# Performance work log

Measured on AMD Instinct MI355X. Metric: run time of the kernel, lower is better.

## Reference

```python
import jax, jax.numpy as jnp
import numpy as np

K, NR, NT, D, NLAYER = 128, 1, 128, 1, 8
PMAX = float(np.power(10.0, 10.0 / 10.0))  # snr=10 dB
SIGMA = 1.0


def _cx(x):
    # [2, ...] real/imag-stacked -> complex
    return x[0] + 1j * x[1]


def _ct(x):
    # conjugate transpose on last two axes
    return jnp.conj(jnp.swapaxes(x, -1, -2))


def _layer(Vc, Hc, up1, up3, up4, wp1, wp3, vp1, vp2, vp4):
    # Vc: [K,Nt,d] complex, Hc: [K,Nr,Nt] complex; params complex, batched over K.
    cdt = Vc.dtype
    I_nr = jnp.eye(NR, dtype=cdt)
    I_d = jnp.eye(D, dtype=cdt)
    I_nt = jnp.eye(NT, dtype=cdt)
    # ---- A_update: A_i = sigma/Pmax * sum_j tr(V_j V_j^H) * I + H_i (sum_j V_j V_j^H) H_i^H
    tr_vv = jnp.einsum('knd,knd->', Vc, jnp.conj(Vc))          # complex scalar
    S = jnp.einsum('knd,kmd->nm', Vc, jnp.conj(Vc))            # [Nt,Nt]
    A = (SIGMA / PMAX) * tr_vv * I_nr + jnp.einsum('krt,tm,ksm->krs', Hc, S, jnp.conj(Hc))  # [K,Nr,Nr]
    # ---- U layer: A_inv_i = p1_i inv(A_i) + 0.01 p3_i ; U_i = A_inv_i H_i V_i + p4_i
    A_inv = up1 @ jnp.linalg.inv(A) + 0.01 * up3
    Un = A_inv @ Hc @ Vc + up4                                  # [K,Nr,d]
    # ---- E_update: E_i = I - U_i^H H_i V_i
    E = I_d - _ct(Un) @ Hc @ Vc                                 # [K,d,d]
    # ---- W layer: W_i = 0.1 p1_i inv(E_i) + 0.01 p3_i
    Wn = 0.1 * (wp1 @ jnp.linalg.inv(E)) + 0.01 * wp3           # [K,d,d]
    # ---- B_update: B = sigma/Pmax * sum_i tr(U_i W_i U_i^H) * I + sum_i H_i^H U_i W_i U_i^H H_i (same for all users)
    UWU = Un @ Wn @ _ct(Un)                                     # [K,Nr,Nr]
    tr_uwu = jnp.trace(UWU, axis1=-2, axis2=-1).sum()
    B = (SIGMA / PMAX) * tr_uwu * I_nt + jnp.sum(_ct(Hc) @ UWU @ Hc, axis=0)  # [Nt,Nt]
    B_inv = jnp.linalg.inv(B)
    # ---- V
    if vp2 is None:  # FinalV: V_i = inv(B) H_i^H U_i W_i
        Vn = (B_inv @ _ct(Hc)) @ Un @ Wn
    else:            # V layer: B_inv_i = p2_i inv(B) + 0.01 p4_i ; V_i = B_inv_i H_i^H U_i W_i + p1_i
        Bm = vp2 @ B_inv + 0.01 * vp4
        Vn = Bm @ _ct(Hc) @ Un @ Wn + vp1
    # ---- Normalize: scale by sqrt(Pmax)/sqrt(Re sum_j tr(V_j V_j^H))
    pw = jnp.sqrt(jnp.real(jnp.einsum('knd,knd->', Vn, jnp.conj(Vn))))
    return (jnp.sqrt(PMAX) / pw) * Vn


def setup_inputs() -> dict:
    key = jax.random.key(0)
    ks = jax.random.split(key, 20)
    f32 = jnp.float32
    def rn(k, shape, scale):
        return (scale * jax.random.normal(k, shape)).astype(f32)
    inp = {
        'V': rn(ks[0], (2, K, NT, D), 1.0),
        'H': rn(ks[1], (2, K, NR, NT), 1.0),
        # mid-layer params, stacked over layers: only params actually used in forward
        'mid_u_p1': rn(ks[2], (NLAYER, 2, K, NR, NR), 0.001),
        'mid_u_p3': rn(ks[3], (NLAYER, 2, K, NR, NR), 0.01),
        'mid_u_p4': rn(ks[4], (NLAYER, 2, K, NR, D), 0.01),
        'mid_w_p1': rn(ks[5], (NLAYER, 2, K, D, D), 0.001),
        'mid_w_p3': rn(ks[6], (NLAYER, 2, K, D, D), 0.01),
        'mid_v_p1': rn(ks[7], (NLAYER, 2, K, NT, D), 0.001),
        'mid_v_p2': rn(ks[8], (NLAYER, 2, K, NT, NT), 0.01),
        'mid_v_p4': rn(ks[9], (NLAYER, 2, K, NT, NT), 0.01),
        # final layer (U + W only)
        'fin_u_p1': rn(ks[10], (2, K, NR, NR), 0.001),
        'fin_u_p3': rn(ks[11], (2, K, NR, NR), 0.01),
        'fin_u_p4': rn(ks[12], (2, K, NR, D), 0.01),
        'fin_w_p1': rn(ks[13], (2, K, D, D), 0.001),
        'fin_w_p3': rn(ks[14], (2, K, D, D), 0.01),
    }
    return inp


def reference(V, H, mid_u_p1, mid_u_p3, mid_u_p4, mid_w_p1, mid_w_p3,
              mid_v_p1, mid_v_p2, mid_v_p4,
              fin_u_p1, fin_u_p3, fin_u_p4, fin_w_p1, fin_w_p3):
    Vc = _cx(V)
    Hc = _cx(H)
    n = mid_u_p1.shape[0]
    for l in range(n):
        Vc = _layer(Vc, Hc,
                    _cx(mid_u_p1[l]), _cx(mid_u_p3[l]), _cx(mid_u_p4[l]),
                    _cx(mid_w_p1[l]), _cx(mid_w_p3[l]),
                    _cx(mid_v_p1[l]), _cx(mid_v_p2[l]), _cx(mid_v_p4[l]))
    Vc = _layer(Vc, Hc,
                _cx(fin_u_p1), _cx(fin_u_p3), _cx(fin_u_p4),
                _cx(fin_w_p1), _cx(fin_w_p3), None, None, None)
    return jnp.stack([jnp.real(Vc), jnp.imag(Vc)]).astype(jnp.float32)
```

## Files before the change

kernel.cpp:

```cpp
#include <hip/hip_runtime.h>
#include <math.h>

#define KK 128
#define NTT 128
#define PMAXF 10.0f
#define SP 0.1f
#define LUT 512
#define LDA 129

typedef float2 c32;

__device__ __forceinline__ c32 cmul(c32 a, c32 b){
    return make_float2(a.x*b.x - a.y*b.y, a.x*b.y + a.y*b.x);
}
__device__ __forceinline__ c32 cmulc(c32 a, c32 b){
    return make_float2(a.x*b.x + a.y*b.y, a.y*b.x - a.x*b.y);
}
__device__ __forceinline__ c32 cinv(c32 a){
    float d = 1.0f/(a.x*a.x + a.y*a.y);
    return make_float2(a.x*d, -a.y*d);
}

__global__ void k_trvv(const float* __restrict__ V0, float* __restrict__ out){
    float s = 0.f;
    for (int e = blockIdx.x*blockDim.x + threadIdx.x; e < 2*KK*NTT; e += gridDim.x*blockDim.x){
        float v = V0[e]; s += v*v;
    }
    __shared__ float red[4];
    for (int d = 32; d; d >>= 1) s += __shfl_down(s, d);
    int lane = threadIdx.x & 63, w = threadIdx.x >> 6;
    if (!lane) red[w] = s;
    __syncthreads();
    if (!threadIdx.x){
        float t = red[0] + red[1] + red[2] + red[3];
        atomicAdd(out, t);
    }
}

__global__ void k_stage1(const float* __restrict__ Hre, const float* __restrict__ Him,
                         const float* __restrict__ V0re, const float* __restrict__ V0im,
                         const float2* __restrict__ VN, int use_vn,
                         const float* __restrict__ pw2prev,
                         const float* __restrict__ trvvp,
                         const float* __restrict__ u1, const float* __restrict__ u3,
                         const float* __restrict__ u4, const float* __restrict__ w1,
                         const float* __restrict__ w3,
                         float* __restrict__ wre, float* __restrict__ wim,
                         float* __restrict__ sre, float* __restrict__ sim,
                         float* __restrict__ sumw)
{
    int k = blockIdx.x, j = threadIdx.x;
    __shared__ float hre_s[NTT], him_s[NTT];
    __shared__ float redq[NTT];
    __shared__ c32 pkk_s;
    hre_s[j] = Hre[k*NTT + j];
    him_s[j] = Him[k*NTT + j];
    __syncthreads();

    float g = 1.0f;
    if (pw2prev) g = sqrtf(PMAXF / *pw2prev);

    float pre = 0.f, pim = 0.f;
    if (use_vn){
        const float2* vr = VN + j*NTT;
        #pragma unroll 4
        for (int n = 0; n < NTT; n++){
            float2 v = vr[n];
            pre += hre_s[n]*v.x - him_s[n]*v.y;
            pim += hre_s[n]*v.y + him_s[n]*v.x;
        }
    } else {
        const float* vr = V0re + j*NTT;
        const float* vi = V0im + j*NTT;
        #pragma unroll 4
        for (int n = 0; n < NTT; n++){
            float a = vr[n], b = vi[n];
            pre += hre_s[n]*a - him_s[n]*b;
            pim += hre_s[n]*b + him_s[n]*a;
        }
    }
    pre *= g; pim *= g;
    if (j == k) pkk_s = make_float2(pre, pim);
    redq[j] = pre*pre + pim*pim;
    __syncthreads();
    for (int d = 64; d; d >>= 1){
        if (j < d) redq[j] += redq[j + d];
        __syncthreads();
    }
    if (j == 0){
        float trvv = pw2prev ? PMAXF : *trvvp;
        float A = SP*trvv + redq[0];
        float invA = 1.0f/A;
        c32 p1 = make_float2(u1[k], u1[KK + k]);
        c32 p3 = make_float2(u3[k], u3[KK + k]);
        c32 p4 = make_float2(u4[k], u4[KK + k]);
        c32 Ainv = make_float2(p1.x*invA + 0.01f*p3.x, p1.y*invA + 0.01f*p3.y);
        c32 Pkk = pkk_s;
        c32 U = cmul(Ainv, Pkk); U.x += p4.x; U.y += p4.y;
        c32 t = cmulc(Pkk, U);
        c32 E = make_float2(1.0f - t.x, -t.y);
        c32 iE = cinv(E);
        c32 q1 = make_float2(w1[k], w1[KK + k]);
        c32 q3 = make_float2(w3[k], w3[KK + k]);
        c32 W = cmul(q1, iE);
        W.x = 0.1f*W.x + 0.01f*q3.x;
        W.y = 0.1f*W.y + 0.01f*q3.y;
        float u2 = U.x*U.x + U.y*U.y;
        c32 wk = make_float2(u2*W.x, u2*W.y);
        c32 sk = cmul(U, W);
        wre[k] = wk.x; wim[k] = wk.y;
        sre[k] = sk.x; sim[k] = sk.y;
        atomicAdd(&sumw[0], wk.x);
        atomicAdd(&sumw[1], wk.y);
    }
}

__global__ void k_bbuild(const float* __restrict__ Hre, const float* __restrict__ Him,
                         const float* __restrict__ wre, const float* __restrict__ wim,
                         const float* __restrict__ sumw, float2* __restrict__ B)
{
    int n = blockIdx.x, m = threadIdx.x;
    __shared__ float cr[KK], ci[KK];
    {
        int k = m;
        c32 h = make_float2(Hre[k*NTT + n], -Him[k*NTT + n]);
        c32 wk = make_float2(wre[k], wim[k]);
        c32 t = cmul(h, wk);
        cr[k] = t.x; ci[k] = t.y;
    }
    __syncthreads();
    float br = 0.f, bi = 0.f;
    #pragma unroll 4
    for (int k = 0; k < KK; k++){
        float hr = Hre[k*NTT + m], hi = Him[k*NTT + m];
        br += cr[k]*hr - ci[k]*hi;
        bi += cr[k]*hi + ci[k]*hr;
    }
    if (n == m){ br += SP*sumw[0]; bi += SP*sumw[1]; }
    B[n*NTT + m] = make_float2(br, bi);
}

__global__ void __launch_bounds__(512, 1) k_lu3(const float2* __restrict__ B,
                                                float2* __restrict__ BT,
                                                float2* __restrict__ rcg,
                                                int* __restrict__ permg)
{
    extern __shared__ float2 As[];
    __shared__ float2 rc_s[KK];
    __shared__ float2 Msc[112*16];
    int t = threadIdx.x;

    for (int e = t; e < KK*NTT; e += LUT){
        int r = e >> 7, c = e & 127;
        As[r*LDA + c] = B[e];
    }
    __syncthreads();

    for (int j = 0; j < 8; ++j){
        const int J0 = j*16;
        for (int ii = 0; ii < 16; ++ii){
            const int gi = J0 + ii;
            float2 piv = As[gi*LDA + gi];
            float2 rc = cinv(piv);
            if (t == 0) rc_s[gi] = rc;
            const int w = 15 - ii;
            const int nel = (127 - gi) * w;
            for (int e = t; e < nel; e += LUT){
                int r = gi + 1 + e / w;
                int c = gi + 1 + e % w;
                float2 m = cmul(As[r*LDA + gi], rc);
                float2 u = As[gi*LDA + c];
                float2 a = As[r*LDA + c];
                a.x -= m.x*u.x - m.y*u.y;
                a.y -= m.x*u.y + m.y*u.x;
                As[r*LDA + c] = a;
            }
            __syncthreads();
        }
        if (j == 7) break;
        const int T0 = J0 + 16;
        const int Rt = 128 - T0;

        for (int e = t; e < Rt*16; e += LUT){
            int rp = e >> 4, i = e & 15;
            float2 l = As[(T0 + rp)*LDA + J0 + i];
            Msc[rp*16 + i] = cmul(l, rc_s[J0 + i]);
        }
        if (t < Rt){
            int c = T0 + t;
            float2 u[16];
            #pragma unroll
            for (int a2 = 0; a2 < 16; ++a2) u[a2] = As[(J0 + a2)*LDA + c];
            #pragma unroll
            for (int a2 = 1; a2 < 16; ++a2){
                #pragma unroll
                for (int i = 0; i < 16; ++i){
                    if (i < a2){
                        float2 m = cmul(As[(J0 + a2)*LDA + J0 + i], rc_s[J0 + i]);
                        u[a2].x -= m.x*u[i].x - m.y*u[i].y;
                        u[a2].y -= m.x*u[i].y + m.y*u[i].x;
                    }
                }
            }
            #pragma unroll
            for (int a2 = 1; a2 < 16; ++a2) As[(J0 + a2)*LDA + c] = u[a2];
        }
        __syncthreads();

        {
            int cl = t & 127;
            int g  = t >> 7;
            if (cl < Rt){
                int c = T0 + cl;
                float2 u[16];
                #pragma unroll
                for (int i = 0; i < 16; ++i) u[i] = As[(J0 + i)*LDA + c];
                for (int r = T0 + g; r < 128; r += 4){
                    int rp = r - T0;
                    float2 a = As[r*LDA + c];
                    #pragma unroll
                    for (int i = 0; i < 16; ++i){
                        float2 m = Msc[rp*16 + i];
                        a.x -= m.x*u[i].x - m.y*u[i].y;
                        a.y -= m.x*u[i].y + m.y*u[i].x;
                    }
                    As[r*LDA + c] = a;
                }
            }
        }
        __syncthreads();
    }

    for (int e = t; e < KK*NTT; e += LUT){
        int c = e >> 7, r = e & 127;
        BT[e] = As[r*LDA + c];
    }
    if (t < KK){ rcg[t] = rc_s[t]; permg[t] = t; }
}

__global__ void k_solve(const float2* __restrict__ BT, const float2* __restrict__ rcg,
                        const int* __restrict__ permg,
                        const float* __restrict__ Hre, const float* __restrict__ Him,
                        float2* __restrict__ X)
{
    int c = blockIdx.x;
    int lane = threadIdx.x;
    __shared__ float2 rc_s[KK];
    rc_s[lane] = rcg[lane];
    rc_s[lane + 64] = rcg[lane + 64];
    int r0 = lane, r1 = lane + 64;
    int o0 = permg[r0], o1 = permg[r1];
    float2 b0 = make_float2(Hre[c*NTT + o0], -Him[c*NTT + o0]);
    float2 b1 = make_float2(Hre[c*NTT + o1], -Him[c*NTT + o1]);
    __syncthreads();

    float2 cur0[8], cur1[8];
    #pragma unroll
    for (int jj = 0; jj < 8; jj++){ cur0[jj] = BT[jj*NTT + r0]; cur1[jj] = BT[jj*NTT + r1]; }
    for (int ib = 0; ib < 16; ib++){
        float2 n0[8], n1[8];
        if (ib < 15){
            int nb = (ib + 1)*8;
            #pragma unroll
            for (int jj = 0; jj < 8; jj++){ n0[jj] = BT[(nb + jj)*NTT + r0]; n1[jj] = BT[(nb + jj)*NTT + r1]; }
        }
        #pragma unroll
        for (int jj = 0; jj < 8; jj++){
            int i = ib*8 + jj;
            float xr, xi;
            if (i < 64){ xr = __shfl(b0.x, i);      xi = __shfl(b0.y, i); }
            else       { xr = __shfl(b1.x, i - 64); xi = __shfl(b1.y, i - 64); }
            float2 rc = rc_s[i];
            float tr = rc.x*xr - rc.y*xi, ti = rc.x*xi + rc.y*xr;
            float2 l0 = cur0[jj], l1 = cur1[jj];
            if (r0 > i){ b0.x -= l0.x*tr - l0.y*ti; b0.y -= l0.x*ti + l0.y*tr; }
            if (r1 > i){ b1.x -= l1.x*tr - l1.y*ti; b1.y -= l1.x*ti + l1.y*tr; }
        }
        if (ib < 15){
            #pragma unroll
            for (int jj = 0; jj < 8; jj++){ cur0[jj] = n0[jj]; cur1[jj] = n1[jj]; }
        }
    }
    #pragma unroll
    for (int jj = 0; jj < 8; jj++){ cur0[jj] = BT[(120 + jj)*NTT + r0]; cur1[jj] = BT[(120 + jj)*NTT + r1]; }
    for (int ib = 15; ib >= 0; ib--){
        float2 n0[8], n1[8];
        if (ib > 0){
            int nb = (ib - 1)*8;
            #pragma unroll
            for (int jj = 0; jj < 8; jj++){ n0[jj] = BT[(nb + jj)*NTT + r0]; n1[jj] = BT[(nb + jj)*NTT + r1]; }
        }
        #pragma unroll
        for (int jj = 7; jj >= 0; jj--){
            int i = ib*8 + jj;
            float yr, yi;
            if (i < 64){ yr = __shfl(b0.x, i);      yi = __shfl(b0.y, i); }
            else       { yr = __shfl(b1.x, i - 64); yi = __shfl(b1.y, i - 64); }
            float2 rc = rc_s[i];
            float xr = rc.x*yr - rc.y*yi, xi = rc.x*yi + rc.y*yr;
            if (r0 == i){ b0.x = xr; b0.y = xi; }
            if (r1 == i){ b1.x = xr; b1.y = xi; }
            float2 u0 = cur0[jj], u1v = cur1[jj];
            if (r0 < i){ b0.x -= u0.x*xr - u0.y*xi; b0.y -= u0.x*xi + u0.y*xr; }
            if (r1 < i){ b1.x -= u1v.x*xr - u1v.y*xi; b1.y -= u1v.x*xi + u1v.y*xr; }
        }
        if (ib > 0){
            #pragma unroll
            for (int jj = 0; jj < 8; jj++){ cur0[jj] = n0[jj]; cur1[jj] = n1[jj]; }
        }
    }
    X[c*NTT + r0] = b0;
    X[c*NTT + r1] = b1;
}

__global__ void k_matvec(const float* __restrict__ p2re, const float* __restrict__ p2im,
                         const float* __restrict__ p4re, const float* __restrict__ p4im,
                         const float2* __restrict__ X,
                         const float* __restrict__ Hre, const float* __restrict__ Him,
                         float2* __restrict__ Y, float2* __restrict__ Z)
{
    int b = blockIdx.x;
    int k = b >> 1, rh = b & 1;
    int t = threadIdx.x;
    __shared__ float2 xv[NTT], hv[NTT];
    if (t < NTT){
        xv[t] = X[k*NTT + t];
        hv[t] = make_float2(Hre[k*NTT + t], -Him[k*NTT + t]);
    }
    __syncthreads();
    int which = t >> 7, u = t & 127;
    int row = rh*64 + (u >> 1), ch = u & 1;
    size_t base = (size_t)k*16384 + (size_t)row*128 + (size_t)ch*64;
    const float* mre = (which ? p4re : p2re) + base;
    const float* mim = (which ? p4im : p2im) + base;
    const float2* vv = (which ? hv : xv) + ch*64;
    float ar = 0.f, ai = 0.f;
    #pragma unroll 4
    for (int cidx = 0; cidx < 64; cidx++){
        float r_ = mre[cidx], i_ = mim[cidx];
        float2 v = vv[cidx];
        ar += r_*v.x - i_*v.y;
        ai += r_*v.y + i_*v.x;
    }
    ar += __shfl_xor(ar, 1);
    ai += __shfl_xor(ai, 1);
    if (ch == 0){
        (which ? Z : Y)[k*NTT + row] = make_float2(ar, ai);
    }
}

__global__ void k_combine(const float2* __restrict__ Y, const float2* __restrict__ Z,
                          const float* __restrict__ sre, const float* __restrict__ sim,
                          const float* __restrict__ p1re, const float* __restrict__ p1im,
                          float2* __restrict__ VN, float* __restrict__ pw2)
{
    float acc = 0.f;
    for (int e = blockIdx.x*blockDim.x + threadIdx.x; e < KK*NTT; e += gridDim.x*blockDim.x){
        int k = e >> 7;
        c32 s = make_float2(sre[k], sim[k]);
        float2 y = Y[e], z = Z[e];
        y.x += 0.01f*z.x; y.y += 0.01f*z.y;
        c32 v = cmul(s, y);
        v.x += p1re[e]; v.y += p1im[e];
        VN[e] = v;
        acc += v.x*v.x + v.y*v.y;
    }
    __shared__ float red[4];
    for (int d = 32; d; d >>= 1) acc += __shfl_down(acc, d);
    int lane = threadIdx.x & 63, w = threadIdx.x >> 6;
    if (!lane) red[w] = acc;
    __syncthreads();
    if (!threadIdx.x) atomicAdd(pw2, red[0] + red[1] + red[2] + red[3]);
}

__global__ void k_finout(const float2* __restrict__ X,
                         const float* __restrict__ sre, const float* __restrict__ sim,
                         float2* __restrict__ VN, float* __restrict__ pw2)
{
    float acc = 0.f;
    for (int e = blockIdx.x*blockDim.x + threadIdx.x; e < KK*NTT; e += gridDim.x*blockDim.x){
        int k = e >> 7;
        c32 s = make_float2(sre[k], sim[k]);
        c32 v = cmul(s, X[e]);
        VN[e] = v;
        acc += v.x*v.x + v.y*v.y;
    }
    __shared__ float red[4];
    for (int d = 32; d; d >>= 1) acc += __shfl_down(acc, d);
    int lane = threadIdx.x & 63, w = threadIdx.x >> 6;
    if (!lane) red[w] = acc;
    __syncthreads();
    if (!threadIdx.x) atomicAdd(pw2, red[0] + red[1] + red[2] + red[3]);
}

__global__ void k_write(const float2* __restrict__ VN, const float* __restrict__ pw2,
                        float* __restrict__ out)
{
    float gsc = sqrtf(PMAXF / *pw2);
    for (int e = blockIdx.x*blockDim.x + threadIdx.x; e < KK*NTT; e += gridDim.x*blockDim.x){
        float2 v = VN[e];
        out[e] = gsc*v.x;
        out[KK*NTT + e] = gsc*v.y;
    }
}

extern "C" void kernel_launch(void* const* d_in, const int* in_sizes, int n_in,
                              void* d_out, int out_size, void* d_ws, size_t ws_size,
                              hipStream_t stream)
{
    const float* V0  = (const float*)d_in[0];
    const float* H   = (const float*)d_in[1];
    const float* mu1 = (const float*)d_in[2];
    const float* mu3 = (const float*)d_in[3];
    const float* mu4 = (const float*)d_in[4];
    const float* mw1 = (const float*)d_in[5];
    const float* mw3 = (const float*)d_in[6];
    const float* mv1 = (const float*)d_in[7];
    const float* mv2 = (const float*)d_in[8];
    const float* mv4 = (const float*)d_in[9];
    const float* fu1 = (const float*)d_in[10];
    const float* fu3 = (const float*)d_in[11];
    const float* fu4 = (const float*)d_in[12];
    const float* fw1 = (const float*)d_in[13];
    const float* fw3 = (const float*)d_in[14];

    float* ws = (float*)d_ws;
    float*  acc  = ws;
    float*  wre  = ws + 64;
    float*  wim  = ws + 192;
    float*  sre  = ws + 320;
    float*  sim  = ws + 448;
    float2* B    = (float2*)(ws + 1024);
    float2* rc   = (float2*)(ws + 33792);
    int*    perm = (int*)  (ws + 34048);
    float2* X    = (float2*)(ws + 34176);
    float2* Y    = (float2*)(ws + 66944);
    float2* Z    = (float2*)(ws + 99712);
    float2* VN   = (float2*)(ws + 132480);
    float2* BT   = (float2*)(ws + 165248);

    const int LU_LDS = KK*LDA*sizeof(float2);
    (void)hipFuncSetAttribute((const void*)k_lu3,
                              hipFuncAttributeMaxDynamicSharedMemorySize, LU_LDS);

    hipMemsetAsync(ws, 0, 64*sizeof(float), stream);
    k_trvv<<<64, 256, 0, stream>>>(V0, ws + 40);

    const float* Hre = H;
    const float* Him = H + 16384;

    for (int l = 0; l < 9; l++){
        bool fin = (l == 8);
        const float* u1 = fin ? fu1 : mu1 + (size_t)l*256;
        const float* u3 = fin ? fu3 : mu3 + (size_t)l*256;
        const float* u4 = fin ? fu4 : mu4 + (size_t)l*256;
        const float* w1 = fin ? fw1 : mw1 + (size_t)l*256;
        const float* w3 = fin ? fw3 : mw3 + (size_t)l*256;

        k_stage1<<<128, 128, 0, stream>>>(Hre, Him, V0, V0 + 16384, VN, (l > 0) ? 1 : 0,
                                          (l > 0) ? (acc + (l - 1)*4 + 2) : nullptr,
                                          ws + 40,
                                          u1, u3, u4, w1, w3,
                                          wre, wim, sre, sim, acc + l*4);
        k_bbuild<<<128, 128, 0, stream>>>(Hre, Him, wre, wim, acc + l*4, B);
        k_lu3<<<1, 512, LU_LDS, stream>>>(B, BT, rc, perm);
        k_solve<<<128, 64, 0, stream>>>(BT, rc, perm, Hre, Him, X);

        if (!fin){
            const float* p2 = mv2 + (size_t)l*4194304;
            const float* p4 = mv4 + (size_t)l*4194304;
            const float* p1 = mv1 + (size_t)l*32768;
            k_matvec<<<256, 256, 0, stream>>>(p2, p2 + 2097152, p4, p4 + 2097152,
                                              X, Hre, Him, Y, Z);
            k_combine<<<64, 256, 0, stream>>>(Y, Z, sre, sim, p1, p1 + 16384,
                                              VN, acc + l*4 + 2);
        } else {
            k_finout<<<64, 256, 0, stream>>>(X, sre, sim, VN, acc + l*4 + 2);
            k_write<<<64, 256, 0, stream>>>(VN, acc + l*4 + 2, (float*)d_out);
        }
    }
}
```

Baseline: 1.767 ms.

## Overlap p4·H matvec with LU, register-blocked panel LU, fuse matvec with combine

The single-block LU kernel gains 128 extra blocks that compute the independent p4·H^H matvec while block 0 factorises, hiding that bandwidth-bound work behind the serial LU. The LU itself is rewritten: the panel factorisation runs in registers with wave shuffles instead of 16 barrier-separated passes, the U-row triangular update is split across 4 lanes per column with shuffle reductions, and the trailing update uses 4x4 register tiles. The p2·X matvec is fused with the combine and power reduction, removing the Y round trip and one launch. The cost is higher register pressure in the LU block and more complex indexing.

```diff
diff --git a/kernel.cpp b/kernel.cpp
--- a/kernel.cpp
+++ b/kernel.cpp
@@ -140,15 +140,46 @@
     B[n*NTT + m] = make_float2(br, bi);
 }
 
-__global__ void __launch_bounds__(512, 1) k_lu3(const float2* __restrict__ B,
+__global__ void __launch_bounds__(512, 1) k_lu4(const float2* __restrict__ B,
                                                 float2* __restrict__ BT,
                                                 float2* __restrict__ rcg,
-                                                int* __restrict__ permg)
-{
+                                                int* __restrict__ permg,
+                                                const float* __restrict__ p4re,
+                                                const float* __restrict__ p4im,
+                                                const float* __restrict__ Hre,
+                                                const float* __restrict__ Him,
+                                                float2* __restrict__ Z)
+{
+    if (blockIdx.x > 0){
+        int k = blockIdx.x - 1;
+        int t = threadIdx.x;
+        int r = t >> 2, q = t & 3;
+        const float* mre = p4re + (size_t)k*16384 + (size_t)r*128 + q*32;
+        const float* mim = p4im + (size_t)k*16384 + (size_t)r*128 + q*32;
+        const float* hr4 = Hre + k*NTT + q*32;
+        const float* hi4 = Him + k*NTT + q*32;
+        float ar = 0.f, ai = 0.f;
+        #pragma unroll
+        for (int ii = 0; ii < 8; ++ii){
+            float4 a = *(const float4*)(mre + 4*ii);
+            float4 b = *(const float4*)(mim + 4*ii);
+            float4 hr = *(const float4*)(hr4 + 4*ii);
+            float4 hi = *(const float4*)(hi4 + 4*ii);
+            ar += a.x*hr.x + b.x*hi.x;  ai += b.x*hr.x - a.x*hi.x;
+            ar += a.y*hr.y + b.y*hi.y;  ai += b.y*hr.y - a.y*hi.y;
+            ar += a.z*hr.z + b.z*hi.z;  ai += b.z*hr.z - a.z*hi.z;
+            ar += a.w*hr.w + b.w*hi.w;  ai += b.w*hr.w - a.w*hi.w;
+        }
+        ar += __shfl_xor(ar, 1); ai += __shfl_xor(ai, 1);
+        ar += __shfl_xor(ar, 2); ai += __shfl_xor(ai, 2);
+        if (q == 0) Z[k*NTT + r] = make_float2(ar, ai);
+        return;
+    }
+
     extern __shared__ float2 As[];
     __shared__ float2 rc_s[KK];
     __shared__ float2 Msc[112*16];
-    int t = threadIdx.x;
+    const int t = threadIdx.x;
 
     for (int e = t; e < KK*NTT; e += LUT){
         int r = e >> 7, c = e & 127;
@@ -157,74 +188,141 @@
     __syncthreads();
 
     for (int j = 0; j < 8; ++j){
-        const int J0 = j*16;
-        for (int ii = 0; ii < 16; ++ii){
-            const int gi = J0 + ii;
-            float2 piv = As[gi*LDA + gi];
-            float2 rc = cinv(piv);
-            if (t == 0) rc_s[gi] = rc;
-            const int w = 15 - ii;
-            const int nel = (127 - gi) * w;
-            for (int e = t; e < nel; e += LUT){
-                int r = gi + 1 + e / w;
-                int c = gi + 1 + e % w;
-                float2 m = cmul(As[r*LDA + gi], rc);
-                float2 u = As[gi*LDA + c];
-                float2 a = As[r*LDA + c];
-                a.x -= m.x*u.x - m.y*u.y;
-                a.y -= m.x*u.y + m.y*u.x;
-                As[r*LDA + c] = a;
-            }
-            __syncthreads();
-        }
+        const int J0 = j*16, T0 = J0 + 16, Rt = 128 - T0;
+
+        if (t < 64){
+            const int l = t;
+            const int r0 = J0 + l, r1 = J0 + 64 + l;
+            const bool h0 = (r0 < 128), h1 = (r1 < 128);
+            float2 a0[16], a1[16];
+            #pragma unroll
+            for (int c = 0; c < 16; ++c){ a0[c] = make_float2(0.f,0.f); a1[c] = make_float2(0.f,0.f); }
+            if (h0){
+                #pragma unroll
+                for (int c = 0; c < 16; ++c) a0[c] = As[r0*LDA + J0 + c];
+            }
+            if (h1){
+                #pragma unroll
+                for (int c = 0; c < 16; ++c) a1[c] = As[r1*LDA + J0 + c];
+            }
+            #pragma unroll
+            for (int ii = 0; ii < 16; ++ii){
+                float2 piv;
+                piv.x = __shfl(a0[ii].x, ii);
+                piv.y = __shfl(a0[ii].y, ii);
+                float2 rc = cinv(piv);
+                if (l == ii) rc_s[J0 + ii] = rc;
+                float2 m0 = cmul(a0[ii], rc);
+                float2 m1 = cmul(a1[ii], rc);
+                const bool act0 = h0 && (l > ii);
+                #pragma unroll
+                for (int c = ii + 1; c < 16; ++c){
+                    float ux = __shfl(a0[c].x, ii);
+                    float uy = __shfl(a0[c].y, ii);
+                    if (act0){
+                        a0[c].x -= m0.x*ux - m0.y*uy;
+                        a0[c].y -= m0.x*uy + m0.y*ux;
+                    }
+                    if (h1){
+                        a1[c].x -= m1.x*ux - m1.y*uy;
+                        a1[c].y -= m1.x*uy + m1.y*ux;
+                    }
+                }
+            }
+            if (h0){
+                #pragma unroll
+                for (int c = 0; c < 16; ++c) As[r0*LDA + J0 + c] = a0[c];
+            }
+            if (h1){
+                #pragma unroll
+                for (int c = 0; c < 16; ++c) As[r1*LDA + J0 + c] = a1[c];
+            }
+        }
+        __syncthreads();
+
         if (j == 7) break;
-        const int T0 = J0 + 16;
-        const int Rt = 128 - T0;
 
         for (int e = t; e < Rt*16; e += LUT){
             int rp = e >> 4, i = e & 15;
-            float2 l = As[(T0 + rp)*LDA + J0 + i];
-            Msc[rp*16 + i] = cmul(l, rc_s[J0 + i]);
-        }
-        if (t < Rt){
-            int c = T0 + t;
-            float2 u[16];
-            #pragma unroll
-            for (int a2 = 0; a2 < 16; ++a2) u[a2] = As[(J0 + a2)*LDA + c];
-            #pragma unroll
-            for (int a2 = 1; a2 < 16; ++a2){
-                #pragma unroll
-                for (int i = 0; i < 16; ++i){
-                    if (i < a2){
-                        float2 m = cmul(As[(J0 + a2)*LDA + J0 + i], rc_s[J0 + i]);
-                        u[a2].x -= m.x*u[i].x - m.y*u[i].y;
-                        u[a2].y -= m.x*u[i].y + m.y*u[i].x;
+            Msc[e] = cmul(As[(T0 + rp)*LDA + J0 + i], rc_s[J0 + i]);
+        }
+        {
+            int q = t & 3, cidx = t >> 2;
+            if (cidx < Rt){
+                int c = T0 + cidx;
+                float2 uq[4];
+                #pragma unroll
+                for (int kk = 0; kk < 4; ++kk) uq[kk] = As[(J0 + q + 4*kk)*LDA + c];
+                #pragma unroll
+                for (int a2 = 1; a2 < 16; ++a2){
+                    float2 part = make_float2(0.f, 0.f);
+                    #pragma unroll
+                    for (int kk = 0; kk < 4; ++kk){
+                        int i = q + 4*kk;
+                        if (i < a2){
+                            float2 mm = cmul(As[(J0 + a2)*LDA + J0 + i], rc_s[J0 + i]);
+                            float2 p = cmul(mm, uq[kk]);
+                            part.x += p.x; part.y += p.y;
+                        }
+                    }
+                    part.x += __shfl_xor(part.x, 1); part.y += __shfl_xor(part.y, 1);
+                    part.x += __shfl_xor(part.x, 2); part.y += __shfl_xor(part.y, 2);
+                    if (q == (a2 & 3)){
+                        uq[a2 >> 2].x -= part.x;
+                        uq[a2 >> 2].y -= part.y;
                     }
                 }
-            }
-            #pragma unroll
-            for (int a2 = 1; a2 < 16; ++a2) As[(J0 + a2)*LDA + c] = u[a2];
+                #pragma unroll
+                for (int kk = 0; kk < 4; ++kk){
+                    int i = q + 4*kk;
+                    if (i != 0) As[(J0 + i)*LDA + c] = uq[kk];
+                }
+            }
         }
         __syncthreads();
 
         {
-            int cl = t & 127;
-            int g  = t >> 7;
-            if (cl < Rt){
-                int c = T0 + cl;
-                float2 u[16];
-                #pragma unroll
-                for (int i = 0; i < 16; ++i) u[i] = As[(J0 + i)*LDA + c];
-                for (int r = T0 + g; r < 128; r += 4){
-                    int rp = r - T0;
-                    float2 a = As[r*LDA + c];
+            int rt = t & 31, cw = t >> 5;
+            if (rt < (Rt >> 2)){
+                int r0 = T0 + rt*4;
+                float2 m[4][16];
+                #pragma unroll
+                for (int s = 0; s < 4; ++s){
+                    const float4* mp = (const float4*)&Msc[(rt*4 + s)*16];
+                    #pragma unroll
+                    for (int hh = 0; hh < 8; ++hh){
+                        float4 v = mp[hh];
+                        m[s][2*hh]   = make_float2(v.x, v.y);
+                        m[s][2*hh+1] = make_float2(v.z, v.w);
+                    }
+                }
+                for (int c0 = T0 + cw*4; c0 < 128; c0 += 64){
+                    float2 acc[4][4];
+                    #pragma unroll
+                    for (int s = 0; s < 4; ++s)
+                        #pragma unroll
+                        for (int cc = 0; cc < 4; ++cc)
+                            acc[s][cc] = As[(r0 + s)*LDA + c0 + cc];
                     #pragma unroll
                     for (int i = 0; i < 16; ++i){
-                        float2 m = Msc[rp*16 + i];
-                        a.x -= m.x*u[i].x - m.y*u[i].y;
-                        a.y -= m.x*u[i].y + m.y*u[i].x;
+                        float2 u0 = As[(J0 + i)*LDA + c0];
+                        float2 u1 = As[(J0 + i)*LDA + c0 + 1];
+                        float2 u2 = As[(J0 + i)*LDA + c0 + 2];
+                        float2 u3 = As[(J0 + i)*LDA + c0 + 3];
+                        #pragma unroll
+                        for (int s = 0; s < 4; ++s){
+                            float2 mm = m[s][i];
+                            acc[s][0].x -= mm.x*u0.x - mm.y*u0.y; acc[s][0].y -= mm.x*u0.y + mm.y*u0.x;
+                            acc[s][1].x -= mm.x*u1.x - mm.y*u1.y; acc[s][1].y -= mm.x*u1.y + mm.y*u1.x;
+                            acc[s][2].x -= mm.x*u2.x - mm.y*u2.y; acc[s][2].y -= mm.x*u2.y + mm.y*u2.x;
+                            acc[s][3].x -= mm.x*u3.x - mm.y*u3.y; acc[s][3].y -= mm.x*u3.y + mm.y*u3.x;
+                        }
                     }
-                    As[r*LDA + c] = a;
+                    #pragma unroll
+                    for (int s = 0; s < 4; ++s)
+                        #pragma unroll
+                        for (int cc = 0; cc < 4; ++cc)
+                            As[(r0 + s)*LDA + c0 + cc] = acc[s][cc];
                 }
             }
         }
@@ -313,64 +411,55 @@
     X[c*NTT + r1] = b1;
 }
 
-__global__ void k_matvec(const float* __restrict__ p2re, const float* __restrict__ p2im,
-                         const float* __restrict__ p4re, const float* __restrict__ p4im,
-                         const float2* __restrict__ X,
-                         const float* __restrict__ Hre, const float* __restrict__ Him,
-                         float2* __restrict__ Y, float2* __restrict__ Z)
-{
-    int b = blockIdx.x;
-    int k = b >> 1, rh = b & 1;
+__global__ void k_mvcomb(const float* __restrict__ p2re, const float* __restrict__ p2im,
+                         const float2* __restrict__ X, const float2* __restrict__ Z,
+                         const float* __restrict__ sre, const float* __restrict__ sim,
+                         const float* __restrict__ p1re, const float* __restrict__ p1im,
+                         float2* __restrict__ VN, float* __restrict__ pw2)
+{
+    int k = blockIdx.x;
     int t = threadIdx.x;
-    __shared__ float2 xv[NTT], hv[NTT];
-    if (t < NTT){
-        xv[t] = X[k*NTT + t];
-        hv[t] = make_float2(Hre[k*NTT + t], -Him[k*NTT + t]);
-    }
-    __syncthreads();
-    int which = t >> 7, u = t & 127;
-    int row = rh*64 + (u >> 1), ch = u & 1;
-    size_t base = (size_t)k*16384 + (size_t)row*128 + (size_t)ch*64;
-    const float* mre = (which ? p4re : p2re) + base;
-    const float* mim = (which ? p4im : p2im) + base;
-    const float2* vv = (which ? hv : xv) + ch*64;
+    __shared__ float2 xv[NTT];
+    __shared__ float red[8];
+    if (t < NTT) xv[t] = X[k*NTT + t];
+    __syncthreads();
+    int r = t >> 2, q = t & 3;
+    const float* mre = p2re + (size_t)k*16384 + (size_t)r*128 + q*32;
+    const float* mim = p2im + (size_t)k*16384 + (size_t)r*128 + q*32;
     float ar = 0.f, ai = 0.f;
-    #pragma unroll 4
-    for (int cidx = 0; cidx < 64; cidx++){
-        float r_ = mre[cidx], i_ = mim[cidx];
-        float2 v = vv[cidx];
-        ar += r_*v.x - i_*v.y;
-        ai += r_*v.y + i_*v.x;
-    }
-    ar += __shfl_xor(ar, 1);
-    ai += __shfl_xor(ai, 1);
-    if (ch == 0){
-        (which ? Z : Y)[k*NTT + row] = make_float2(ar, ai);
-    }
-}
-
-__global__ void k_combine(const float2* __restrict__ Y, const float2* __restrict__ Z,
-                          const float* __restrict__ sre, const float* __restrict__ sim,
-                          const float* __restrict__ p1re, const float* __restrict__ p1im,
-                          float2* __restrict__ VN, float* __restrict__ pw2)
-{
-    float acc = 0.f;
-    for (int e = blockIdx.x*blockDim.x + threadIdx.x; e < KK*NTT; e += gridDim.x*blockDim.x){
-        int k = e >> 7;
+    #pragma unroll
+    for (int ii = 0; ii < 8; ++ii){
+        float4 a = *(const float4*)(mre + 4*ii);
+        float4 b = *(const float4*)(mim + 4*ii);
+        float2 x0 = xv[q*32 + 4*ii], x1 = xv[q*32 + 4*ii + 1];
+        float2 x2 = xv[q*32 + 4*ii + 2], x3 = xv[q*32 + 4*ii + 3];
+        ar += a.x*x0.x - b.x*x0.y;  ai += a.x*x0.y + b.x*x0.x;
+        ar += a.y*x1.x - b.y*x1.y;  ai += a.y*x1.y + b.y*x1.x;
+        ar += a.z*x2.x - b.z*x2.y;  ai += a.z*x2.y + b.z*x2.x;
+        ar += a.w*x3.x - b.w*x3.y;  ai += a.w*x3.y + b.w*x3.x;
+    }
+    ar += __shfl_xor(ar, 1); ai += __shfl_xor(ai, 1);
+    ar += __shfl_xor(ar, 2); ai += __shfl_xor(ai, 2);
+    float pwl = 0.f;
+    if (q == 0){
+        float2 z = Z[k*NTT + r];
         c32 s = make_float2(sre[k], sim[k]);
-        float2 y = Y[e], z = Z[e];
-        y.x += 0.01f*z.x; y.y += 0.01f*z.y;
+        float2 y = make_float2(ar + 0.01f*z.x, ai + 0.01f*z.y);
         c32 v = cmul(s, y);
-        v.x += p1re[e]; v.y += p1im[e];
-        VN[e] = v;
-        acc += v.x*v.x + v.y*v.y;
-    }
-    __shared__ float red[4];
-    for (int d = 32; d; d >>= 1) acc += __shfl_down(acc, d);
-    int lane = threadIdx.x & 63, w = threadIdx.x >> 6;
-    if (!lane) red[w] = acc;
-    __syncthreads();
-    if (!threadIdx.x) atomicAdd(pw2, red[0] + red[1] + red[2] + red[3]);
+        v.x += p1re[k*NTT + r]; v.y += p1im[k*NTT + r];
+        VN[k*NTT + r] = v;
+        pwl = v.x*v.x + v.y*v.y;
+    }
+    for (int d = 32; d; d >>= 1) pwl += __shfl_down(pwl, d);
+    int lane = t & 63, w = t >> 6;
+    if (!lane) red[w] = pwl;
+    __syncthreads();
+    if (!t){
+        float tt = 0.f;
+        #pragma unroll
+        for (int w2 = 0; w2 < 8; ++w2) tt += red[w2];
+        atomicAdd(pw2, tt);
+    }
 }
 
 __global__ void k_finout(const float2* __restrict__ X,
@@ -434,13 +523,12 @@
     float2* rc   = (float2*)(ws + 33792);
     int*    perm = (int*)  (ws + 34048);
     float2* X    = (float2*)(ws + 34176);
-    float2* Y    = (float2*)(ws + 66944);
     float2* Z    = (float2*)(ws + 99712);
     float2* VN   = (float2*)(ws + 132480);
     float2* BT   = (float2*)(ws + 165248);
 
     const int LU_LDS = KK*LDA*sizeof(float2);
-    (void)hipFuncSetAttribute((const void*)k_lu3,
+    (void)hipFuncSetAttribute((const void*)k_lu4,
                               hipFuncAttributeMaxDynamicSharedMemorySize, LU_LDS);
 
     hipMemsetAsync(ws, 0, 64*sizeof(float), stream);
@@ -463,18 +551,21 @@
                                           u1, u3, u4, w1, w3,
                                           wre, wim, sre, sim, acc + l*4);
         k_bbuild<<<128, 128, 0, stream>>>(Hre, Him, wre, wim, acc + l*4, B);
-        k_lu3<<<1, 512, LU_LDS, stream>>>(B, BT, rc, perm);
-        k_solve<<<128, 64, 0, stream>>>(BT, rc, perm, Hre, Him, X);
 
         if (!fin){
+            const float* p4 = mv4 + (size_t)l*4194304;
+            k_lu4<<<129, 512, LU_LDS, stream>>>(B, BT, rc, perm,
+                                                p4, p4 + 2097152, Hre, Him, Z);
+            k_solve<<<128, 64, 0, stream>>>(BT, rc, perm, Hre, Him, X);
             const float* p2 = mv2 + (size_t)l*4194304;
-            const float* p4 = mv4 + (size_t)l*4194304;
             const float* p1 = mv1 + (size_t)l*32768;
-            k_matvec<<<256, 256, 0, stream>>>(p2, p2 + 2097152, p4, p4 + 2097152,
-                                              X, Hre, Him, Y, Z);
-            k_combine<<<64, 256, 0, stream>>>(Y, Z, sre, sim, p1, p1 + 16384,
+            k_mvcomb<<<128, 512, 0, stream>>>(p2, p2 + 2097152, X, Z,
+                                              sre, sim, p1, p1 + 16384,
                                               VN, acc + l*4 + 2);
         } else {
+            k_lu4<<<1, 512, LU_LDS, stream>>>(B, BT, rc, perm,
+                                              nullptr, nullptr, Hre, Him, Z);
+            k_solve<<<128, 64, 0, stream>>>(BT, rc, perm, Hre, Him, X);
             k_finout<<<64, 256, 0, stream>>>(X, sre, sim, VN, acc + l*4 + 2);
             k_write<<<64, 256, 0, stream>>>(VN, acc + l*4 + 2, (float*)d_out);
         }
```

New measurement: 3.509 ms. 1.99x slower.
